# Kernel tuning notes

Measured on AMD Instinct MI355X. Metric: run time of the kernel, lower is better.

Reference implementation:

```python
import jax, jax.numpy as jnp
import numpy as np

S_CNT, R_CNT, P_CNT = 10000, 10000, 50000
K_S, K_R, K_P = 64, 64, 128
T = 50
N = 1_000_000


def setup_inputs() -> dict:
    key = jax.random.key(0)
    ks, kr, kp, kt, kws, kwr, kwp = jax.random.split(key, 7)
    s = jax.random.randint(ks, (N,), 0, S_CNT)
    r = jax.random.randint(kr, (N,), 0, R_CNT)
    p = jax.random.randint(kp, (N,), 0, P_CNT)
    t = jax.random.randint(kt, (N,), 0, T)
    X = jnp.stack([s, r, p, t], axis=1).astype(jnp.int64)  # n x 4
    # xavier_uniform-like init: bound = sqrt(6/(fan_in+fan_out))
    def xavier(k, shape):
        bound = np.sqrt(6.0 / (shape[0] + shape[1])).astype(np.float32)
        return jax.random.uniform(k, shape, jnp.float32, -bound, bound)
    s_embeds = xavier(kws, (T * S_CNT, K_S))
    r_embeds = xavier(kwr, (T * R_CNT, K_R))
    p_embeds = xavier(kwp, (P_CNT, K_P))
    return {"X": X, "s_embeds": s_embeds, "r_embeds": r_embeds, "p_embeds": p_embeds}


def reference(X, s_embeds, r_embeds, p_embeds):
    s, r, p, t = X[:, 0], X[:, 1], X[:, 2], X[:, 3]
    st = s + t * S_CNT
    rt = r + t * R_CNT
    se = s_embeds[st]            # [n, K_S]
    re = r_embeds[rt]            # [n, K_R]
    pe = p_embeds[p]             # [n, K_S + K_R]
    # dot(concat(se, re), pe) without materializing the concat
    prod = jnp.sum(se * pe[:, :K_S], axis=1) + jnp.sum(re * pe[:, K_S:], axis=1)
    return jax.nn.sigmoid(prod)  # [n]
```

## Files before the change

### kernel.cpp

```cpp
#include <hip/hip_runtime.h>
#include <cstdint>

#define S_CNT 10000
#define R_CNT 10000

__global__ __launch_bounds__(256) void srct_kernel(
    const int* __restrict__ X,
    const float* __restrict__ s_embeds,
    const float* __restrict__ r_embeds,
    const float* __restrict__ p_embeds,
    float* __restrict__ out, int n)
{
    const int g = threadIdx.x >> 4;
    const int l = threadIdx.x & 15;
    const int i = blockIdx.x * 16 + g;
    if (i >= n) return;

    const int4 xi = *reinterpret_cast<const int4*>(X + 4ll * i);
    const int s = xi.x, r = xi.y, p = xi.z, t = xi.w;

    const long long st = (long long)s + (long long)t * S_CNT;
    const long long rt = (long long)r + (long long)t * R_CNT;

    const float4 se = *reinterpret_cast<const float4*>(s_embeds + st * 64 + l * 4);
    const float4 pl = *reinterpret_cast<const float4*>(p_embeds + (long long)p * 128 + l * 4);
    const float4 re = *reinterpret_cast<const float4*>(r_embeds + rt * 64 + l * 4);
    const float4 ph = *reinterpret_cast<const float4*>(p_embeds + (long long)p * 128 + 64 + l * 4);

    float acc = se.x * pl.x + se.y * pl.y + se.z * pl.z + se.w * pl.w
              + re.x * ph.x + re.y * ph.y + re.z * ph.z + re.w * ph.w;

    acc += __shfl_xor(acc, 1, 64);
    acc += __shfl_xor(acc, 2, 64);
    acc += __shfl_xor(acc, 4, 64);
    acc += __shfl_xor(acc, 8, 64);

    if (l == 0) {
        out[i] = 1.0f / (1.0f + __expf(-acc));
    }
}

extern "C" void kernel_launch(void* const* d_in, const int* in_sizes, int n_in,
                              void* d_out, int out_size, void* d_ws, size_t ws_size,
                              hipStream_t stream) {
    const int*   X        = (const int*)d_in[0];
    const float* s_embeds = (const float*)d_in[1];
    const float* r_embeds = (const float*)d_in[2];
    const float* p_embeds = (const float*)d_in[3];
    float* out = (float*)d_out;

    const int n = in_sizes[0] / 4;
    const int blocks = (n + 15) / 16;
    srct_kernel<<<blocks, 256, 0, stream>>>(X, s_embeds, r_embeds, p_embeds, out, n);
}
```

Baseline: 138.7 us.

## Bin queries by time bucket before gathering embeddings for cache locality

Adds a pass that counts queries per time index and scatters them into per-time buckets in workspace, then a dot kernel handles each bucket's queries together. Because every query in a bucket reads the same 10000-row slice of the s and r embedding tables, the gathered rows should stay in cache better. The cost is two extra launches, a scatter write and re-read of the packed indices, and global atomics. Buckets that overflow fall back to a scalar in-place computation, and the original direct kernel runs when the workspace is too small.

Result: slower. 172.6 us (+24.5%).

```diff
diff --git a/kernel.cpp b/kernel.cpp
--- a/kernel.cpp
+++ b/kernel.cpp
@@ -3,8 +3,116 @@
 
 #define S_CNT 10000
 #define R_CNT 10000
+#define NBUCKET 50
+#define CAP 21504
+#define CURS 16
+#define NSLOT (NBUCKET * CAP)
+#define CUR_INTS (64 * CURS)
+#define IDX_OFF_INTS CUR_INTS
+#define PACKED_OFF_BYTES (4096 + 4 * NSLOT)
+#define WS_NEED ((size_t)PACKED_OFF_BYTES + 16ull * NSLOT)
 
-__global__ __launch_bounds__(256) void srct_kernel(
+__global__ __launch_bounds__(256) void zero_kernel(int* __restrict__ ws) {
+    ws[blockIdx.x * 256 + threadIdx.x] = 0;
+}
+
+__global__ __launch_bounds__(256) void bin_kernel(
+    const int* __restrict__ X, int n, int* __restrict__ ws,
+    const float* __restrict__ se, const float* __restrict__ re,
+    const float* __restrict__ pe, float* __restrict__ out)
+{
+    __shared__ int lhist[NBUCKET], lbase[NBUCKET], lcur[NBUCKET];
+    int* cursors = ws;
+    int* idxArr  = ws + IDX_OFF_INTS;
+    int4* packed = reinterpret_cast<int4*>(reinterpret_cast<char*>(ws) + PACKED_OFF_BYTES);
+
+    const int tid = threadIdx.x;
+    const long long base = (long long)blockIdx.x * 1024;
+    if (tid < NBUCKET) lhist[tid] = 0;
+    __syncthreads();
+
+    int4 xs[4];
+    #pragma unroll
+    for (int it = 0; it < 4; ++it) {
+        const long long i = base + it * 256 + tid;
+        if (i < n) {
+            xs[it] = *reinterpret_cast<const int4*>(X + 4 * i);
+            atomicAdd(&lhist[xs[it].w], 1);
+        } else {
+            xs[it].w = -1;
+        }
+    }
+    __syncthreads();
+    if (tid < NBUCKET) {
+        const int c = lhist[tid];
+        lbase[tid] = c ? atomicAdd(&cursors[tid * CURS], c) : 0;
+        lcur[tid] = 0;
+    }
+    __syncthreads();
+    #pragma unroll
+    for (int it = 0; it < 4; ++it) {
+        const int t = xs[it].w;
+        if (t < 0) continue;
+        const long long i = base + it * 256 + tid;
+        const int rank = lbase[t] + atomicAdd(&lcur[t], 1);
+        if (rank < CAP) {
+            const int gidx = t * CAP + rank;
+            packed[gidx] = xs[it];
+            idxArr[gidx] = (int)i;
+        } else {
+            const long long st = (long long)xs[it].x + (long long)t * S_CNT;
+            const long long rt = (long long)xs[it].y + (long long)t * R_CNT;
+            const long long p  = xs[it].z;
+            float acc = 0.f;
+            for (int k = 0; k < 64; ++k)
+                acc += se[st * 64 + k] * pe[p * 128 + k]
+                     + re[rt * 64 + k] * pe[p * 128 + 64 + k];
+            out[i] = 1.0f / (1.0f + __expf(-acc));
+        }
+    }
+}
+
+__global__ __launch_bounds__(256) void dot_kernel(
+    const int* __restrict__ ws,
+    const float* __restrict__ s_embeds,
+    const float* __restrict__ r_embeds,
+    const float* __restrict__ p_embeds,
+    float* __restrict__ out)
+{
+    const int g = threadIdx.x >> 4;
+    const int l = threadIdx.x & 15;
+    const int j = blockIdx.x * 16 + g;
+    if (j >= NSLOT) return;
+    const unsigned bucket = (unsigned)j / CAP;
+    const unsigned rank   = (unsigned)j - bucket * CAP;
+    const int cnt = ws[bucket * CURS];
+    if (rank >= (unsigned)cnt) return;
+
+    const int4 pk = reinterpret_cast<const int4*>(
+        reinterpret_cast<const char*>(ws) + PACKED_OFF_BYTES)[j];
+    const int i = ws[IDX_OFF_INTS + j];
+
+    const long long st = (long long)pk.x + (long long)pk.w * S_CNT;
+    const long long rt = (long long)pk.y + (long long)pk.w * R_CNT;
+    const long long p  = pk.z;
+
+    const float4 se = *reinterpret_cast<const float4*>(s_embeds + st * 64 + l * 4);
+    const float4 re = *reinterpret_cast<const float4*>(r_embeds + rt * 64 + l * 4);
+    const float4 pl = *reinterpret_cast<const float4*>(p_embeds + p * 128 + l * 4);
+    const float4 ph = *reinterpret_cast<const float4*>(p_embeds + p * 128 + 64 + l * 4);
+
+    float acc = se.x * pl.x + se.y * pl.y + se.z * pl.z + se.w * pl.w
+              + re.x * ph.x + re.y * ph.y + re.z * ph.z + re.w * ph.w;
+
+    acc += __shfl_xor(acc, 1, 64);
+    acc += __shfl_xor(acc, 2, 64);
+    acc += __shfl_xor(acc, 4, 64);
+    acc += __shfl_xor(acc, 8, 64);
+
+    if (l == 0) out[i] = 1.0f / (1.0f + __expf(-acc));
+}
+
+__global__ __launch_bounds__(256) void direct_kernel(
     const int* __restrict__ X,
     const float* __restrict__ s_embeds,
     const float* __restrict__ r_embeds,
@@ -15,29 +123,21 @@
     const int l = threadIdx.x & 15;
     const int i = blockIdx.x * 16 + g;
     if (i >= n) return;
-
     const int4 xi = *reinterpret_cast<const int4*>(X + 4ll * i);
-    const int s = xi.x, r = xi.y, p = xi.z, t = xi.w;
-
-    const long long st = (long long)s + (long long)t * S_CNT;
-    const long long rt = (long long)r + (long long)t * R_CNT;
-
+    const long long st = (long long)xi.x + (long long)xi.w * S_CNT;
+    const long long rt = (long long)xi.y + (long long)xi.w * R_CNT;
+    const long long p  = xi.z;
     const float4 se = *reinterpret_cast<const float4*>(s_embeds + st * 64 + l * 4);
-    const float4 pl = *reinterpret_cast<const float4*>(p_embeds + (long long)p * 128 + l * 4);
     const float4 re = *reinterpret_cast<const float4*>(r_embeds + rt * 64 + l * 4);
-    const float4 ph = *reinterpret_cast<const float4*>(p_embeds + (long long)p * 128 + 64 + l * 4);
-
+    const float4 pl = *reinterpret_cast<const float4*>(p_embeds + p * 128 + l * 4);
+    const float4 ph = *reinterpret_cast<const float4*>(p_embeds + p * 128 + 64 + l * 4);
     float acc = se.x * pl.x + se.y * pl.y + se.z * pl.z + se.w * pl.w
               + re.x * ph.x + re.y * ph.y + re.z * ph.z + re.w * ph.w;
-
     acc += __shfl_xor(acc, 1, 64);
     acc += __shfl_xor(acc, 2, 64);
     acc += __shfl_xor(acc, 4, 64);
     acc += __shfl_xor(acc, 8, 64);
-
-    if (l == 0) {
-        out[i] = 1.0f / (1.0f + __expf(-acc));
-    }
+    if (l == 0) out[i] = 1.0f / (1.0f + __expf(-acc));
 }
 
 extern "C" void kernel_launch(void* const* d_in, const int* in_sizes, int n_in,
@@ -48,8 +148,18 @@
     const float* r_embeds = (const float*)d_in[2];
     const float* p_embeds = (const float*)d_in[3];
     float* out = (float*)d_out;
+    const int n = in_sizes[0] / 4;
 
-    const int n = in_sizes[0] / 4;
-    const int blocks = (n + 15) / 16;
-    srct_kernel<<<blocks, 256, 0, stream>>>(X, s_embeds, r_embeds, p_embeds, out, n);
+    if (ws_size < WS_NEED) {
+        direct_kernel<<<(n + 15) / 16, 256, 0, stream>>>(
+            X, s_embeds, r_embeds, p_embeds, out, n);
+        return;
+    }
+
+    int* ws = (int*)d_ws;
+    zero_kernel<<<CUR_INTS / 256, 256, 0, stream>>>(ws);
+    bin_kernel<<<(n + 1023) / 1024, 256, 0, stream>>>(
+        X, n, ws, s_embeds, r_embeds, p_embeds, out);
+    dot_kernel<<<(NSLOT + 15) / 16, 256, 0, stream>>>(
+        ws, s_embeds, r_embeds, p_embeds, out);
 }
```

## Bucket rows by p-group and stage p_embeds tiles in LDS

Applied to the files above, without the earlier changes.

Replaces the single gather kernel with a counting-sort pipeline: histogram, scan and scatter the rows into buckets keyed by p-row group, time step and s-half. A compute kernel then loads each group's 98-row p_embeds slab into shared memory once and serves all of its rows from LDS, with the s/r gathers better localised by t. The aim is to remove repeated random global reads of the 128-float p rows. The cost is four extra kernel launches, atomics over 1M rows, a 16-byte-per-row packed buffer, and a single-block scan that serialises 64K bins. The compute grid is only 512 blocks with skewed per-group work.

After: 274.4 us. 1.98x slower.

```diff
diff --git a/kernel.cpp b/kernel.cpp
--- a/kernel.cpp
+++ b/kernel.cpp
@@ -3,41 +3,149 @@
 
 #define S_CNT 10000
 #define R_CNT 10000
+#define NT 50
+#define PG 512
+#define PROWS 98
+#define KEYS_PER_G 128
+#define NBINS (PG * KEYS_PER_G)
+#define PACKED_OFF_B (1 << 20)
 
-__global__ __launch_bounds__(256) void srct_kernel(
+__global__ __launch_bounds__(256) void zero_kernel(int4* __restrict__ cur4) {
+    cur4[blockIdx.x * 256 + threadIdx.x] = make_int4(0, 0, 0, 0);
+}
+
+__global__ __launch_bounds__(256) void hist_kernel(const int* __restrict__ X, int n,
+                                                   int* __restrict__ cursors) {
+    const int i = blockIdx.x * 256 + threadIdx.x;
+    if (i < n) {
+        const int4 x = *reinterpret_cast<const int4*>(X + 4ll * i);
+        const int key = (x.z / PROWS) * KEYS_PER_G + x.w * 2 + (x.x >= 5000);
+        atomicAdd(&cursors[key], 1);
+    }
+}
+
+__global__ __launch_bounds__(1024) void scan_kernel(const int* __restrict__ cursors,
+                                                    int* __restrict__ cursors2,
+                                                    int* __restrict__ offsets, int n) {
+    __shared__ int part[1024];
+    const int tid = threadIdx.x;
+    const int base = tid * (NBINS / 1024);
+    int sum = 0;
+    for (int k = 0; k < NBINS / 1024; ++k) sum += cursors[base + k];
+    part[tid] = sum;
+    __syncthreads();
+    for (int d = 1; d < 1024; d <<= 1) {
+        const int v = (tid >= d) ? part[tid - d] : 0;
+        __syncthreads();
+        part[tid] += v;
+        __syncthreads();
+    }
+    int run = part[tid] - sum;
+    for (int k = 0; k < NBINS / 1024; ++k) {
+        const int c = cursors[base + k];
+        offsets[base + k] = run;
+        cursors2[base + k] = run;
+        run += c;
+    }
+    if (tid == 1023) offsets[NBINS] = run;
+}
+
+__global__ __launch_bounds__(256) void scatter_kernel(const int* __restrict__ X, int n,
+                                                      int* __restrict__ cursors2,
+                                                      int4* __restrict__ packed) {
+    const int i = blockIdx.x * 256 + threadIdx.x;
+    if (i < n) {
+        const int4 x = *reinterpret_cast<const int4*>(X + 4ll * i);
+        const int key = (x.z / PROWS) * KEYS_PER_G + x.w * 2 + (x.x >= 5000);
+        const int pos = atomicAdd(&cursors2[key], 1);
+        packed[pos] = make_int4(x.x | (x.w << 16), x.y, x.z, i);
+    }
+}
+
+__global__ __launch_bounds__(256) void compute_kernel(
+    const int* __restrict__ offsets, const int4* __restrict__ packed,
+    const float* __restrict__ s_embeds, const float* __restrict__ r_embeds,
+    const float* __restrict__ p_embeds, float* __restrict__ out) {
+    __shared__ __align__(16) float plds[PROWS * 128];
+    const int g = blockIdx.x;
+    const int start = offsets[g * KEYS_PER_G];
+    const int end   = offsets[(g + 1) * KEYS_PER_G];
+    if (start >= end) return;
+
+    const int prow0 = g * PROWS;
+    const int rows = min(PROWS, 50000 - prow0);
+    const int nf4 = rows * 32;
+    const float4* src = reinterpret_cast<const float4*>(p_embeds + (long long)prow0 * 128);
+    for (int k = threadIdx.x; k < nf4; k += 256)
+        reinterpret_cast<float4*>(plds)[k] = src[k];
+    __syncthreads();
+
+    const int gl = threadIdx.x >> 4;
+    const int l  = threadIdx.x & 15;
+
+    for (int sb = start; sb < end; sb += 32) {
+        const int jA = sb + gl;
+        const int jB = sb + 16 + gl;
+        const int jAc = min(jA, end - 1);
+        const int jBc = min(jB, end - 1);
+        const int4 a = packed[jAc];
+        const int4 b = packed[jBc];
+
+        const int sA = a.x & 0xFFFF, tA = a.x >> 16;
+        const int sB = b.x & 0xFFFF, tB = b.x >> 16;
+        const int stA = sA + tA * S_CNT, rtA = a.y + tA * R_CNT;
+        const int stB = sB + tB * S_CNT, rtB = b.y + tB * R_CNT;
+
+        const float4 seA = *reinterpret_cast<const float4*>(s_embeds + (long long)stA * 64 + l * 4);
+        const float4 reA = *reinterpret_cast<const float4*>(r_embeds + (long long)rtA * 64 + l * 4);
+        const float4 seB = *reinterpret_cast<const float4*>(s_embeds + (long long)stB * 64 + l * 4);
+        const float4 reB = *reinterpret_cast<const float4*>(r_embeds + (long long)rtB * 64 + l * 4);
+
+        const int pA = (a.z - prow0) * 128;
+        const int pB = (b.z - prow0) * 128;
+        const float4 plA = *reinterpret_cast<const float4*>(plds + pA + l * 4);
+        const float4 phA = *reinterpret_cast<const float4*>(plds + pA + 64 + l * 4);
+        const float4 plB = *reinterpret_cast<const float4*>(plds + pB + l * 4);
+        const float4 phB = *reinterpret_cast<const float4*>(plds + pB + 64 + l * 4);
+
+        float accA = seA.x * plA.x + seA.y * plA.y + seA.z * plA.z + seA.w * plA.w
+                   + reA.x * phA.x + reA.y * phA.y + reA.z * phA.z + reA.w * phA.w;
+        float accB = seB.x * plB.x + seB.y * plB.y + seB.z * plB.z + seB.w * plB.w
+                   + reB.x * phB.x + reB.y * phB.y + reB.z * phB.z + reB.w * phB.w;
+
+        accA += __shfl_xor(accA, 1, 64);  accB += __shfl_xor(accB, 1, 64);
+        accA += __shfl_xor(accA, 2, 64);  accB += __shfl_xor(accB, 2, 64);
+        accA += __shfl_xor(accA, 4, 64);  accB += __shfl_xor(accB, 4, 64);
+        accA += __shfl_xor(accA, 8, 64);  accB += __shfl_xor(accB, 8, 64);
+
+        if (l == 0 && jA < end) out[a.w] = 1.0f / (1.0f + __expf(-accA));
+        if (l == 0 && jB < end) out[b.w] = 1.0f / (1.0f + __expf(-accB));
+    }
+}
+
+__global__ __launch_bounds__(256) void direct_kernel(
     const int* __restrict__ X,
-    const float* __restrict__ s_embeds,
-    const float* __restrict__ r_embeds,
-    const float* __restrict__ p_embeds,
-    float* __restrict__ out, int n)
-{
+    const float* __restrict__ s_embeds, const float* __restrict__ r_embeds,
+    const float* __restrict__ p_embeds, float* __restrict__ out, int n) {
     const int g = threadIdx.x >> 4;
     const int l = threadIdx.x & 15;
     const int i = blockIdx.x * 16 + g;
     if (i >= n) return;
-
     const int4 xi = *reinterpret_cast<const int4*>(X + 4ll * i);
-    const int s = xi.x, r = xi.y, p = xi.z, t = xi.w;
-
-    const long long st = (long long)s + (long long)t * S_CNT;
-    const long long rt = (long long)r + (long long)t * R_CNT;
-
+    const long long st = (long long)xi.x + (long long)xi.w * S_CNT;
+    const long long rt = (long long)xi.y + (long long)xi.w * R_CNT;
+    const long long p  = xi.z;
     const float4 se = *reinterpret_cast<const float4*>(s_embeds + st * 64 + l * 4);
-    const float4 pl = *reinterpret_cast<const float4*>(p_embeds + (long long)p * 128 + l * 4);
     const float4 re = *reinterpret_cast<const float4*>(r_embeds + rt * 64 + l * 4);
-    const float4 ph = *reinterpret_cast<const float4*>(p_embeds + (long long)p * 128 + 64 + l * 4);
-
+    const float4 pl = *reinterpret_cast<const float4*>(p_embeds + p * 128 + l * 4);
+    const float4 ph = *reinterpret_cast<const float4*>(p_embeds + p * 128 + 64 + l * 4);
     float acc = se.x * pl.x + se.y * pl.y + se.z * pl.z + se.w * pl.w
               + re.x * ph.x + re.y * ph.y + re.z * ph.z + re.w * ph.w;
-
     acc += __shfl_xor(acc, 1, 64);
     acc += __shfl_xor(acc, 2, 64);
     acc += __shfl_xor(acc, 4, 64);
     acc += __shfl_xor(acc, 8, 64);
-
-    if (l == 0) {
-        out[i] = 1.0f / (1.0f + __expf(-acc));
-    }
+    if (l == 0) out[i] = 1.0f / (1.0f + __expf(-acc));
 }
 
 extern "C" void kernel_launch(void* const* d_in, const int* in_sizes, int n_in,
@@ -48,8 +156,26 @@
     const float* r_embeds = (const float*)d_in[2];
     const float* p_embeds = (const float*)d_in[3];
     float* out = (float*)d_out;
+    const int n = in_sizes[0] / 4;
 
-    const int n = in_sizes[0] / 4;
-    const int blocks = (n + 15) / 16;
-    srct_kernel<<<blocks, 256, 0, stream>>>(X, s_embeds, r_embeds, p_embeds, out, n);
+    const size_t ws_need = (size_t)PACKED_OFF_B + 16ull * (size_t)n;
+    if (ws_size < ws_need) {
+        direct_kernel<<<(n + 15) / 16, 256, 0, stream>>>(
+            X, s_embeds, r_embeds, p_embeds, out, n);
+        return;
+    }
+
+    int* wsI = (int*)d_ws;
+    int* cursors  = wsI;
+    int* cursors2 = wsI + NBINS;
+    int* offsets  = wsI + 2 * NBINS;
+    int4* packed  = reinterpret_cast<int4*>((char*)d_ws + PACKED_OFF_B);
+
+    const int sgrid = (n + 255) / 256;
+    zero_kernel<<<NBINS / 1024, 256, 0, stream>>>(reinterpret_cast<int4*>(cursors));
+    hist_kernel<<<sgrid, 256, 0, stream>>>(X, n, cursors);
+    scan_kernel<<<1, 1024, 0, stream>>>(cursors, cursors2, offsets, n);
+    scatter_kernel<<<sgrid, 256, 0, stream>>>(X, n, cursors2, packed);
+    compute_kernel<<<PG, 256, 0, stream>>>(
+        offsets, packed, s_embeds, r_embeds, p_embeds, out);
 }
```
